# Optimization experiments

Measured on AMD Instinct MI355X. Metric: run time of the kernel, lower is better.

The kernel has to match this reference:

```python
import jax, jax.numpy as jnp
import numpy as np

VOXEL_SIZE = jnp.array([0.16, 0.16], dtype=jnp.float32)
PC_RANGE = jnp.array([0.0, -39.68], dtype=jnp.float32)
BN_EPS = 1e-3
B, P, M, C_IN = 4, 12000, 32, 4
FEAT_IN = C_IN + 5  # actual concatenated feature width (source code bug: claims +6)
FD = 64


def _bn_train(x, gamma, beta):
    # BatchNorm1d in training mode: stats per channel over all (B*P, M) positions.
    mean = x.mean(axis=(0, 1, 2))
    var = jnp.square(x - mean).mean(axis=(0, 1, 2))  # biased variance
    return (x - mean) * jax.lax.rsqrt(var + BN_EPS) * gamma + beta


def setup_inputs() -> dict:
    key = jax.random.key(0)
    ks = jax.random.split(key, 5)
    voxels = jax.random.normal(ks[0], (B, P, M, C_IN), dtype=jnp.float32)
    voxel_coords = jax.random.randint(ks[1], (B, P, 4), 0, 496, dtype=jnp.int32)
    voxel_num_points = jax.random.randint(ks[2], (B, P), 0, 33, dtype=jnp.int32)
    W1 = jax.random.normal(ks[3], (FEAT_IN, FD), dtype=jnp.float32) * (1.0 / np.sqrt(FEAT_IN))
    W2 = jax.random.normal(ks[4], (FD, FD), dtype=jnp.float32) * (1.0 / np.sqrt(FD))
    g1 = jnp.ones((FD,), jnp.float32); b1 = jnp.zeros((FD,), jnp.float32)
    g2 = jnp.ones((FD,), jnp.float32); b2 = jnp.zeros((FD,), jnp.float32)
    return {"voxels": voxels, "voxel_coords": voxel_coords,
            "voxel_num_points": voxel_num_points,
            "W1": W1, "g1": g1, "b1": b1, "W2": W2, "g2": g2, "b2": b2}


def reference(voxels, voxel_coords, voxel_num_points, W1, g1, b1, W2, g2, b2):
    xyz = voxels[..., :3]                      # (B,P,M,3)
    extra = voxels[..., 3:]                    # (B,P,M,C_IN-3)
    # pillar centers from [x, y] grid indices (coords are [b, z, y, x])
    idx_xy = voxel_coords[..., jnp.array([3, 2])].astype(jnp.float32)  # (B,P,2)
    centers = (idx_xy + 0.5) * VOXEL_SIZE + PC_RANGE                   # (B,P,2)
    offset = xyz[..., :2] - centers[:, :, None, :]                     # (B,P,M,2)
    z_center = xyz[..., 2:3].mean(axis=2, keepdims=True)               # (B,P,1,1)
    centers_exp = jnp.broadcast_to(centers[:, :, None, :], (B, P, M, 2))
    z_exp = jnp.broadcast_to(z_center, (B, P, M, 1))
    f = jnp.concatenate([xyz, extra, offset, centers_exp, z_exp], axis=-1)  # (B,P,M,9)
    # mask out padding points
    mask = (jnp.arange(M)[None, None, :, None] < voxel_num_points[:, :, None, None])
    f = f * mask.astype(f.dtype)
    # PFN layer 1: linear (no bias) -> BN(train) -> ReLU
    h = jax.nn.relu(_bn_train(jnp.einsum('bpmi,io->bpmo', f, W1), g1, b1))
    # PFN layer 2 (last): linear -> BN -> ReLU -> max over points
    h = jax.nn.relu(_bn_train(jnp.einsum('bpmi,io->bpmo', h, W2), g2, b2))
    return h.max(axis=2)  # (B,P,FD)
```

## Files before the change

kernel.cpp:

```cpp
#include <hip/hip_runtime.h>
#include <math.h>

#define NB 4
#define NPI 12000
#define NM 32
#define NPTS (NB*NPI*NM)
#define NPIL (NB*NPI)

#define K1_BLOCKS 1500
#define K1_STRIDE (K1_BLOCKS*256)
#define K1_ITERS 4
#define NMOM 54

#define CHUNK 128
#define NBATCH (NPTS/CHUNK)
#define SB 512

typedef __attribute__((ext_vector_type(8))) short bfrag;
typedef __attribute__((ext_vector_type(16))) float f32x16;


__device__ __forceinline__ void make_f(float4 v, int4 cc, int np, int m, float zc, float f[9]) {
  const float cx = ((float)cc.w + 0.5f) * 0.16f + 0.0f;
  const float cy = ((float)cc.z + 0.5f) * 0.16f - 39.68f;
  f[0] = v.x; f[1] = v.y; f[2] = v.z; f[3] = v.w;
  f[4] = v.x - cx; f[5] = v.y - cy; f[6] = cx; f[7] = cy; f[8] = zc;
  const float msk = (m < np) ? 1.0f : 0.0f;
#pragma unroll
  for (int i = 0; i < 9; ++i) f[i] *= msk;
}


__global__ __launch_bounds__(256) void k_moments(
    const float4* __restrict__ vox, const int4* __restrict__ coords,
    const int* __restrict__ npnts, float* __restrict__ P1) {
  const int t = blockIdx.x * 256 + threadIdx.x;
  float acc[NMOM];
#pragma unroll
  for (int v = 0; v < NMOM; ++v) acc[v] = 0.0f;

#pragma unroll
  for (int j = 0; j < K1_ITERS; ++j) {
    const int pt = t + j * K1_STRIDE;
    const int pil = pt >> 5;
    const int m = pt & 31;
    const float4 v = vox[pt];
    const int4 cc = coords[pil];
    const int np = npnts[pil];
    float z = v.z;
#pragma unroll
    for (int s = 1; s < 32; s <<= 1) z += __shfl_xor(z, s, 32);
    const float zc = z * (1.0f / 32.0f);
    float f[9];
    make_f(v, cc, np, m, zc, f);
    int vi = 0;
#pragma unroll
    for (int i = 0; i < 9; ++i) acc[vi++] += f[i];
#pragma unroll
    for (int i = 0; i < 9; ++i)
#pragma unroll
      for (int jj = i; jj < 9; ++jj) acc[vi++] += f[i] * f[jj];
  }

#pragma unroll
  for (int v = 0; v < NMOM; ++v) {
    float x = acc[v];
#pragma unroll
    for (int s = 1; s < 64; s <<= 1) x += __shfl_xor(x, s, 64);
    acc[v] = x;
  }
  __shared__ float red[4][NMOM];
  const int wave = threadIdx.x >> 6, lane = threadIdx.x & 63;
  if (lane == 0) {
#pragma unroll
    for (int v = 0; v < NMOM; ++v) red[wave][v] = acc[v];
  }
  __syncthreads();
  if (threadIdx.x < NMOM) {
    float s = red[0][threadIdx.x] + red[1][threadIdx.x] + red[2][threadIdx.x] + red[3][threadIdx.x];
    P1[threadIdx.x * K1_BLOCKS + blockIdx.x] = s;
  }
}


__global__ __launch_bounds__(256) void k_rowreduce(
    const float* __restrict__ src, double* __restrict__ dst, int ncols) {
  const int row = blockIdx.x;
  const float* p = src + row * ncols;
  double sd = 0.0;
  for (int i = threadIdx.x; i < ncols; i += 256) sd += (double)p[i];
#pragma unroll
  for (int s = 1; s < 64; s <<= 1) sd += __shfl_xor(sd, s, 64);
  __shared__ double rd[4];
  const int wave = threadIdx.x >> 6, lane = threadIdx.x & 63;
  if (lane == 0) rd[wave] = sd;
  __syncthreads();
  if (threadIdx.x == 0) dst[row] = rd[0] + rd[1] + rd[2] + rd[3];
}


__global__ void k_fin1(const double* __restrict__ T1, const float* __restrict__ W1,
                       const float* __restrict__ g1, const float* __restrict__ b1,
                       float* __restrict__ params) {
  const int c = threadIdx.x;
  double w[9];
#pragma unroll
  for (int i = 0; i < 9; ++i) w[i] = (double)W1[i * 64 + c];
  double mean = 0.0;
#pragma unroll
  for (int i = 0; i < 9; ++i) mean += w[i] * T1[i];
  mean /= (double)NPTS;
  double e2 = 0.0;
  int v = 9;
#pragma unroll
  for (int i = 0; i < 9; ++i)
#pragma unroll
    for (int j = i; j < 9; ++j) {
      const double t = T1[v++] * w[i] * w[j];
      e2 += (i == j) ? t : 2.0 * t;
    }
  e2 /= (double)NPTS;
  const double var = e2 - mean * mean;
  const double a = (double)g1[c] / sqrt(var + 0.001);
  params[c] = (float)a;
  params[64 + c] = (float)((double)b1[c] - mean * a);
}


__global__ __launch_bounds__(256) void k_stats2(
    const float4* __restrict__ vox, const int4* __restrict__ coords,
    const int* __restrict__ npnts, const float* __restrict__ W1,
    const float* __restrict__ W2, const float* __restrict__ g2,
    const float* __restrict__ params, float* __restrict__ P2,
    float* __restrict__ Y2SEL) {
  __shared__ __align__(16) unsigned short W1Thi[64][16];
  __shared__ __align__(16) unsigned short W1Tlo[64][16];
  __shared__ __align__(16) float a1s[64], b1s[64];
  __shared__ __align__(16) unsigned short fhi[128][16];
  __shared__ __align__(16) unsigned short flo[128][16];
  __shared__ __align__(16) unsigned short h1hi[128][64];
  __shared__ __align__(16) unsigned short h1lo[128][64];
  __shared__ __align__(16) unsigned short W2Thi[64][64];
  __shared__ __align__(16) unsigned short W2Tlo[64][64];
  __shared__ float redS[4][64], redQ[4][64];

  const int t = threadIdx.x;
  if (t < 64) { a1s[t] = params[t]; b1s[t] = params[64 + t]; }
  for (int i = t; i < 1024; i += 256) {
    const int c = i >> 4, k = i & 15;
    const float x = (k < 9) ? W1[k * 64 + c] : 0.0f;
    const unsigned int b = __float_as_uint(x);
    W1Thi[c][k] = (unsigned short)(b >> 16);
    const float r = x - __uint_as_float(b & 0xFFFF0000u);
    W1Tlo[c][k] = (unsigned short)(__float_as_uint(r) >> 16);
  }
  for (int i = t; i < 4096; i += 256) {
    const int k = i >> 6, c = i & 63;
    const float x = W2[i];
    const unsigned int b = __float_as_uint(x);
    const float r = x - __uint_as_float(b & 0xFFFF0000u);
    const int kc = k ^ ((c & 7) << 3);
    W2Thi[c][kc] = (unsigned short)(b >> 16);
    W2Tlo[c][kc] = (unsigned short)(__float_as_uint(r) >> 16);
  }

  const int lane = t & 63;
  const int wv = t >> 6;
  const int ch = lane & 31;
  const float sg0 = (g2[ch] >= 0.0f) ? 1.0f : -1.0f;
  const float sg1 = (g2[32 + ch] >= 0.0f) ? 1.0f : -1.0f;
  __syncthreads();

  const int arow = 32 * wv + ch;
  const int koff = 8 * (lane >> 5);
  const int swf = (arow & 1) << 3;
  const int swB = (ch & 7) << 3;
  const float a10 = a1s[ch], b10 = b1s[ch];
  const float a11 = a1s[32 + ch], b11 = b1s[32 + ch];
  const bfrag w1h0 = *(const bfrag*)&W1Thi[ch][koff];
  const bfrag w1l0 = *(const bfrag*)&W1Tlo[ch][koff];
  const bfrag w1h1 = *(const bfrag*)&W1Thi[32 + ch][koff];
  const bfrag w1l1 = *(const bfrag*)&W1Tlo[32 + ch][koff];

  float psum = 0.0f, psq = 0.0f;

  int bb0 = blockIdx.x;
  float4 v = vox[bb0 * CHUNK + 32 * wv + ch];
  int4 cc = coords[bb0 * 4 + wv];
  int np = npnts[bb0 * 4 + wv];

  for (int bb = bb0; bb < NBATCH; bb += SB) {
    float z = v.z;
#pragma unroll
    for (int s = 1; s < 64; s <<= 1) z += __shfl_xor(z, s, 64);
    const float zc = z * (1.0f / 64.0f);
    float f[9];
    make_f(v, cc, np, ch, zc, f);

    {
      const int bbn = bb + SB;
      const int bbs = (bbn < NBATCH) ? bbn : bb;
      v = vox[bbs * CHUNK + 32 * wv + ch];
      cc = coords[bbs * 4 + wv];
      np = npnts[bbs * 4 + wv];
    }

    {
      unsigned int pk[8];
#pragma unroll
      for (int i = 0; i < 8; ++i) pk[i] = 0u;
#pragma unroll
      for (int i = 0; i < 9; ++i) {
        const unsigned int b = __float_as_uint(f[i]);
        const float r = f[i] - __uint_as_float(b & 0xFFFF0000u);
        const unsigned int hi = b >> 16;
        const unsigned int lo = __float_as_uint(r) >> 16;
        const unsigned int part = (lane < 32) ? hi : lo;
        pk[i >> 1] |= part << ((i & 1) * 16);
      }
      unsigned short* dst = (lane < 32) ? &fhi[arow][0] : &flo[arow][0];
      uint4 q0; q0.x = pk[0]; q0.y = pk[1]; q0.z = pk[2]; q0.w = pk[3];
      uint4 q1; q1.x = pk[4]; q1.y = pk[5]; q1.z = pk[6]; q1.w = pk[7];
      *(uint4*)(dst + (0 ^ swf)) = q0;
      *(uint4*)(dst + (8 ^ swf)) = q1;
    }

    f32x16 yA0, yA1;
#pragma unroll
    for (int i = 0; i < 16; ++i) { yA0[i] = 0.0f; yA1[i] = 0.0f; }
    {
      const bfrag fa_hi = *(const bfrag*)&fhi[arow][koff ^ swf];
      const bfrag fa_lo = *(const bfrag*)&flo[arow][koff ^ swf];
      yA0 = __builtin_amdgcn_mfma_f32_32x32x16_bf16(fa_hi, w1h0, yA0, 0, 0, 0);
      yA1 = __builtin_amdgcn_mfma_f32_32x32x16_bf16(fa_hi, w1h1, yA1, 0, 0, 0);
      yA0 = __builtin_amdgcn_mfma_f32_32x32x16_bf16(fa_hi, w1l0, yA0, 0, 0, 0);
      yA1 = __builtin_amdgcn_mfma_f32_32x32x16_bf16(fa_hi, w1l1, yA1, 0, 0, 0);
      yA0 = __builtin_amdgcn_mfma_f32_32x32x16_bf16(fa_lo, w1h0, yA0, 0, 0, 0);
      yA1 = __builtin_amdgcn_mfma_f32_32x32x16_bf16(fa_lo, w1h1, yA1, 0, 0, 0);
    }

    const int rbase = 4 * (lane >> 5);
#pragma unroll
    for (int reg = 0; reg < 16; ++reg) {
      const int pt = (reg & 3) + 8 * (reg >> 2) + rbase;
      const int row = 32 * wv + pt;
      const int swz = (pt & 7) << 3;
      {
        const float h = fmaxf(fmaf(yA0[reg], a10, b10), 0.0f);
        const unsigned int b = __float_as_uint(h);
        const float r = h - __uint_as_float(b & 0xFFFF0000u);
        h1hi[row][ch ^ swz] = (unsigned short)(b >> 16);
        h1lo[row][ch ^ swz] = (unsigned short)(__float_as_uint(r) >> 16);
      }
      {
        const float h = fmaxf(fmaf(yA1[reg], a11, b11), 0.0f);
        const unsigned int b = __float_as_uint(h);
        const float r = h - __uint_as_float(b & 0xFFFF0000u);
        h1hi[row][(32 + ch) ^ swz] = (unsigned short)(b >> 16);
        h1lo[row][(32 + ch) ^ swz] = (unsigned short)(__float_as_uint(r) >> 16);
      }
    }

    f32x16 acc0, acc1;
#pragma unroll
    for (int i = 0; i < 16; ++i) { acc0[i] = 0.0f; acc1[i] = 0.0f; }
    const int swA = (arow & 7) << 3;
#pragma unroll
    for (int ks = 0; ks < 4; ++ks) {
      const int kk = koff + 16 * ks;
      const bfrag ahi = *(const bfrag*)&h1hi[arow][kk ^ swA];
      const bfrag alo = *(const bfrag*)&h1lo[arow][kk ^ swA];
      const bfrag bhi0 = *(const bfrag*)&W2Thi[ch][kk ^ swB];
      const bfrag blo0 = *(const bfrag*)&W2Tlo[ch][kk ^ swB];
      const bfrag bhi1 = *(const bfrag*)&W2Thi[32 + ch][kk ^ swB];
      const bfrag blo1 = *(const bfrag*)&W2Tlo[32 + ch][kk ^ swB];
      acc0 = __builtin_amdgcn_mfma_f32_32x32x16_bf16(ahi, bhi0, acc0, 0, 0, 0);
      acc1 = __builtin_amdgcn_mfma_f32_32x32x16_bf16(ahi, bhi1, acc1, 0, 0, 0);
      acc0 = __builtin_amdgcn_mfma_f32_32x32x16_bf16(ahi, blo0, acc0, 0, 0, 0);
      acc1 = __builtin_amdgcn_mfma_f32_32x32x16_bf16(ahi, blo1, acc1, 0, 0, 0);
      acc0 = __builtin_amdgcn_mfma_f32_32x32x16_bf16(alo, bhi0, acc0, 0, 0, 0);
      acc1 = __builtin_amdgcn_mfma_f32_32x32x16_bf16(alo, bhi1, acc1, 0, 0, 0);
    }

    float s0 = 0, q0 = 0, m0 = -INFINITY, s1 = 0, q1 = 0, m1 = -INFINITY;
#pragma unroll
    for (int i = 0; i < 16; ++i) {
      const float v0 = acc0[i], v1 = acc1[i];
      s0 += v0; q0 = fmaf(v0, v0, q0); m0 = fmaxf(m0, v0 * sg0);
      s1 += v1; q1 = fmaf(v1, v1, q1); m1 = fmaxf(m1, v1 * sg1);
    }
    s0 += __shfl_xor(s0, 32, 64); q0 += __shfl_xor(q0, 32, 64);
    m0 = fmaxf(m0, __shfl_xor(m0, 32, 64));
    s1 += __shfl_xor(s1, 32, 64); q1 += __shfl_xor(q1, 32, 64);
    m1 = fmaxf(m1, __shfl_xor(m1, 32, 64));
    const bool hiHalf = lane >= 32;
    psum += hiHalf ? s1 : s0;
    psq += hiHalf ? q1 : q0;
    Y2SEL[(bb * 4 + wv) * 64 + lane] = hiHalf ? m1 : m0;
  }

  redS[wv][lane] = psum;
  redQ[wv][lane] = psq;
  __syncthreads();
  if (t < 64) {
    const float s = redS[0][t] + redS[1][t] + redS[2][t] + redS[3][t];
    const float q = redQ[0][t] + redQ[1][t] + redQ[2][t] + redQ[3][t];
    P2[t * SB + blockIdx.x] = s;
    P2[(64 + t) * SB + blockIdx.x] = q;
  }
}


__global__ void k_fin2(const double* __restrict__ T2, const float* __restrict__ g2,
                       const float* __restrict__ b2, float* __restrict__ params) {
  const int c = threadIdx.x;
  const double mean = T2[c] / (double)NPTS;
  const double var = T2[64 + c] / (double)NPTS - mean * mean;
  const double a = (double)g2[c] / sqrt(var + 0.001);
  params[128 + c] = (float)a;
  params[192 + c] = (float)((double)b2[c] - mean * a);
}


__global__ __launch_bounds__(256) void k_final(
    const float* __restrict__ params, const float* __restrict__ Y2SEL,
    float* __restrict__ out) {
  const int idx = blockIdx.x * 256 + threadIdx.x;
  const int c = idx & 63;
  const float a2 = params[128 + c];
  const float b2 = params[192 + c];
  const float v = Y2SEL[idx];
  const float sel = (a2 >= 0.0f) ? v : -v;
  out[idx] = fmaxf(fmaf(sel, a2, b2), 0.0f);
}


extern "C" void kernel_launch(void* const* d_in, const int* in_sizes, int n_in,
                              void* d_out, int out_size, void* d_ws, size_t ws_size,
                              hipStream_t stream) {
  const float4* vox = (const float4*)d_in[0];
  const int4* coords = (const int4*)d_in[1];
  const int* npnts = (const int*)d_in[2];
  const float* W1 = (const float*)d_in[3];
  const float* g1 = (const float*)d_in[4];
  const float* b1 = (const float*)d_in[5];
  const float* W2 = (const float*)d_in[6];
  const float* g2 = (const float*)d_in[7];
  const float* b2 = (const float*)d_in[8];
  float* out = (float*)d_out;

  char* w = (char*)d_ws;
  size_t off = 0;
  double* T1 = (double*)(w + off); off += 512;
  double* T2 = (double*)(w + off); off += 1024;
  float* P1 = (float*)(w + off); off += NMOM * K1_BLOCKS * 4;
  float* P2 = (float*)(w + off); off += 128 * SB * 4;
  float* params = (float*)(w + off); off += 256 * 4;
  float* Y2SEL = (float*)(w + off); off += (size_t)NPIL * 64 * 4;

  k_moments<<<K1_BLOCKS, 256, 0, stream>>>(vox, coords, npnts, P1);
  k_rowreduce<<<NMOM, 256, 0, stream>>>(P1, T1, K1_BLOCKS);
  k_fin1<<<1, 64, 0, stream>>>(T1, W1, g1, b1, params);
  k_stats2<<<SB, 256, 0, stream>>>(vox, coords, npnts, W1, W2, g2, params, P2, Y2SEL);
  k_rowreduce<<<128, 256, 0, stream>>>(P2, T2, SB);
  k_fin2<<<1, 64, 0, stream>>>(T2, g2, b2, params);
  k_final<<<(NPIL * 64) / 256, 256, 0, stream>>>(params, Y2SEL, out);
}
```

Measured before the change: 115.8 us.

## Build layer-1 A fragments in registers, pack h1 hi/lo, raise grid size

Layer-1 input fragments are now assembled directly in registers instead of being staged through shared memory. The hi and lo bf16 halves of the hidden activations are packed into one 32-bit LDS array, and the reduction scratch reuses the W1 buffers, which shrinks LDS use per block. The stats2 grid grows from 512 to 768 blocks so more blocks can be resident. The trade-off is extra bit-manipulation ALU work to unpack hi/lo when loading layer-2 operands, plus an extra barrier at the end.

```diff
diff --git a/kernel.cpp b/kernel.cpp
--- a/kernel.cpp
+++ b/kernel.cpp
@@ -14,7 +14,7 @@
 
 #define CHUNK 128
 #define NBATCH (NPTS/CHUNK)
-#define SB 512
+#define SB 768
 
 typedef __attribute__((ext_vector_type(8))) short bfrag;
 typedef __attribute__((ext_vector_type(16))) float f32x16;
@@ -136,13 +136,9 @@
   __shared__ __align__(16) unsigned short W1Thi[64][16];
   __shared__ __align__(16) unsigned short W1Tlo[64][16];
   __shared__ __align__(16) float a1s[64], b1s[64];
-  __shared__ __align__(16) unsigned short fhi[128][16];
-  __shared__ __align__(16) unsigned short flo[128][16];
-  __shared__ __align__(16) unsigned short h1hi[128][64];
-  __shared__ __align__(16) unsigned short h1lo[128][64];
+  __shared__ __align__(16) unsigned int  h1p[128][64];
   __shared__ __align__(16) unsigned short W2Thi[64][64];
   __shared__ __align__(16) unsigned short W2Tlo[64][64];
-  __shared__ float redS[4][64], redQ[4][64];
 
   const int t = threadIdx.x;
   if (t < 64) { a1s[t] = params[t]; b1s[t] = params[64 + t]; }
@@ -173,8 +169,8 @@
 
   const int arow = 32 * wv + ch;
   const int koff = 8 * (lane >> 5);
-  const int swf = (arow & 1) << 3;
   const int swB = (ch & 7) << 3;
+  const int swA = (arow & 7) << 2;
   const float a10 = a1s[ch], b10 = b1s[ch];
   const float a11 = a1s[32 + ch], b11 = b1s[32 + ch];
   const bfrag w1h0 = *(const bfrag*)&W1Thi[ch][koff];
@@ -205,71 +201,73 @@
       np = npnts[bbs * 4 + wv];
     }
 
+    bfrag fa_hi, fa_lo;
     {
-      unsigned int pk[8];
-#pragma unroll
-      for (int i = 0; i < 8; ++i) pk[i] = 0u;
-#pragma unroll
-      for (int i = 0; i < 9; ++i) {
-        const unsigned int b = __float_as_uint(f[i]);
-        const float r = f[i] - __uint_as_float(b & 0xFFFF0000u);
-        const unsigned int hi = b >> 16;
-        const unsigned int lo = __float_as_uint(r) >> 16;
-        const unsigned int part = (lane < 32) ? hi : lo;
-        pk[i >> 1] |= part << ((i & 1) * 16);
+      unsigned int ahw[4] = {0u, 0u, 0u, 0u}, alw[4] = {0u, 0u, 0u, 0u};
+#pragma unroll
+      for (int e = 0; e < 8; ++e) {
+        const float x = (lane < 32) ? f[e] : ((e == 0) ? f[8] : 0.0f);
+        const unsigned int b = __float_as_uint(x);
+        const float r = x - __uint_as_float(b & 0xFFFF0000u);
+        ahw[e >> 1] |= (b >> 16) << ((e & 1) * 16);
+        alw[e >> 1] |= (__float_as_uint(r) >> 16) << ((e & 1) * 16);
       }
-      unsigned short* dst = (lane < 32) ? &fhi[arow][0] : &flo[arow][0];
-      uint4 q0; q0.x = pk[0]; q0.y = pk[1]; q0.z = pk[2]; q0.w = pk[3];
-      uint4 q1; q1.x = pk[4]; q1.y = pk[5]; q1.z = pk[6]; q1.w = pk[7];
-      *(uint4*)(dst + (0 ^ swf)) = q0;
-      *(uint4*)(dst + (8 ^ swf)) = q1;
+      union U { unsigned int u[4]; bfrag b; };
+      U ch_, cl_;
+      ch_.u[0] = ahw[0]; ch_.u[1] = ahw[1]; ch_.u[2] = ahw[2]; ch_.u[3] = ahw[3];
+      cl_.u[0] = alw[0]; cl_.u[1] = alw[1]; cl_.u[2] = alw[2]; cl_.u[3] = alw[3];
+      fa_hi = ch_.b; fa_lo = cl_.b;
     }
 
     f32x16 yA0, yA1;
 #pragma unroll
     for (int i = 0; i < 16; ++i) { yA0[i] = 0.0f; yA1[i] = 0.0f; }
-    {
-      const bfrag fa_hi = *(const bfrag*)&fhi[arow][koff ^ swf];
-      const bfrag fa_lo = *(const bfrag*)&flo[arow][koff ^ swf];
-      yA0 = __builtin_amdgcn_mfma_f32_32x32x16_bf16(fa_hi, w1h0, yA0, 0, 0, 0);
-      yA1 = __builtin_amdgcn_mfma_f32_32x32x16_bf16(fa_hi, w1h1, yA1, 0, 0, 0);
-      yA0 = __builtin_amdgcn_mfma_f32_32x32x16_bf16(fa_hi, w1l0, yA0, 0, 0, 0);
-      yA1 = __builtin_amdgcn_mfma_f32_32x32x16_bf16(fa_hi, w1l1, yA1, 0, 0, 0);
-      yA0 = __builtin_amdgcn_mfma_f32_32x32x16_bf16(fa_lo, w1h0, yA0, 0, 0, 0);
-      yA1 = __builtin_amdgcn_mfma_f32_32x32x16_bf16(fa_lo, w1h1, yA1, 0, 0, 0);
-    }
+    yA0 = __builtin_amdgcn_mfma_f32_32x32x16_bf16(fa_hi, w1h0, yA0, 0, 0, 0);
+    yA1 = __builtin_amdgcn_mfma_f32_32x32x16_bf16(fa_hi, w1h1, yA1, 0, 0, 0);
+    yA0 = __builtin_amdgcn_mfma_f32_32x32x16_bf16(fa_hi, w1l0, yA0, 0, 0, 0);
+    yA1 = __builtin_amdgcn_mfma_f32_32x32x16_bf16(fa_hi, w1l1, yA1, 0, 0, 0);
+    yA0 = __builtin_amdgcn_mfma_f32_32x32x16_bf16(fa_lo, w1h0, yA0, 0, 0, 0);
+    yA1 = __builtin_amdgcn_mfma_f32_32x32x16_bf16(fa_lo, w1h1, yA1, 0, 0, 0);
 
     const int rbase = 4 * (lane >> 5);
 #pragma unroll
     for (int reg = 0; reg < 16; ++reg) {
       const int pt = (reg & 3) + 8 * (reg >> 2) + rbase;
       const int row = 32 * wv + pt;
-      const int swz = (pt & 7) << 3;
+      const int swz = (pt & 7) << 2;
       {
         const float h = fmaxf(fmaf(yA0[reg], a10, b10), 0.0f);
         const unsigned int b = __float_as_uint(h);
         const float r = h - __uint_as_float(b & 0xFFFF0000u);
-        h1hi[row][ch ^ swz] = (unsigned short)(b >> 16);
-        h1lo[row][ch ^ swz] = (unsigned short)(__float_as_uint(r) >> 16);
+        h1p[row][ch ^ swz] = (__float_as_uint(r) & 0xFFFF0000u) | (b >> 16);
       }
       {
         const float h = fmaxf(fmaf(yA1[reg], a11, b11), 0.0f);
         const unsigned int b = __float_as_uint(h);
         const float r = h - __uint_as_float(b & 0xFFFF0000u);
-        h1hi[row][(32 + ch) ^ swz] = (unsigned short)(b >> 16);
-        h1lo[row][(32 + ch) ^ swz] = (unsigned short)(__float_as_uint(r) >> 16);
+        h1p[row][(32 + ch) ^ swz] = (__float_as_uint(r) & 0xFFFF0000u) | (b >> 16);
       }
     }
 
     f32x16 acc0, acc1;
 #pragma unroll
     for (int i = 0; i < 16; ++i) { acc0[i] = 0.0f; acc1[i] = 0.0f; }
-    const int swA = (arow & 7) << 3;
 #pragma unroll
     for (int ks = 0; ks < 4; ++ks) {
       const int kk = koff + 16 * ks;
-      const bfrag ahi = *(const bfrag*)&h1hi[arow][kk ^ swA];
-      const bfrag alo = *(const bfrag*)&h1lo[arow][kk ^ swA];
+      const uint4 pa0 = *(const uint4*)&h1p[arow][(kk) ^ swA];
+      const uint4 pa1 = *(const uint4*)&h1p[arow][(kk + 4) ^ swA];
+      union U { unsigned int u[4]; bfrag b; };
+      U uh, ul;
+      uh.u[0] = ((pa0.y & 0xFFFFu) << 16) | (pa0.x & 0xFFFFu);
+      uh.u[1] = ((pa0.w & 0xFFFFu) << 16) | (pa0.z & 0xFFFFu);
+      uh.u[2] = ((pa1.y & 0xFFFFu) << 16) | (pa1.x & 0xFFFFu);
+      uh.u[3] = ((pa1.w & 0xFFFFu) << 16) | (pa1.z & 0xFFFFu);
+      ul.u[0] = (pa0.y & 0xFFFF0000u) | (pa0.x >> 16);
+      ul.u[1] = (pa0.w & 0xFFFF0000u) | (pa0.z >> 16);
+      ul.u[2] = (pa1.y & 0xFFFF0000u) | (pa1.x >> 16);
+      ul.u[3] = (pa1.w & 0xFFFF0000u) | (pa1.z >> 16);
+      const bfrag ahi = uh.b, alo = ul.b;
       const bfrag bhi0 = *(const bfrag*)&W2Thi[ch][kk ^ swB];
       const bfrag blo0 = *(const bfrag*)&W2Tlo[ch][kk ^ swB];
       const bfrag bhi1 = *(const bfrag*)&W2Thi[32 + ch][kk ^ swB];
@@ -299,12 +297,15 @@
     Y2SEL[(bb * 4 + wv) * 64 + lane] = hiHalf ? m1 : m0;
   }
 
-  redS[wv][lane] = psum;
-  redQ[wv][lane] = psq;
+  __syncthreads();
+  float* redS = (float*)&W1Thi[0][0];
+  float* redQ = (float*)&W1Tlo[0][0];
+  redS[wv * 64 + lane] = psum;
+  redQ[wv * 64 + lane] = psq;
   __syncthreads();
   if (t < 64) {
-    const float s = redS[0][t] + redS[1][t] + redS[2][t] + redS[3][t];
-    const float q = redQ[0][t] + redQ[1][t] + redQ[2][t] + redQ[3][t];
+    const float s = redS[t] + redS[64 + t] + redS[128 + t] + redS[192 + t];
+    const float q = redQ[t] + redQ[64 + t] + redQ[128 + t] + redQ[192 + t];
     P2[t * SB + blockIdx.x] = s;
     P2[(64 + t) * SB + blockIdx.x] = q;
   }
```

New measurement: 120.6 us. +4.1%, slower.
